# Performance work log

Hardware: AMD Instinct MI355X
Metric: run time of the kernel (lower is better)

Reference implementation:

```python
import jax, jax.numpy as jnp
import numpy as np

LEVELS = 2
BASE_BLOCK = (16, 16)
MAX_DIST = 8
IMG = (1024, 1024)


def _to_blocks(x, bh, bw):
    # [N,C,H,W] -> [BX,BY,N,C,bh,bw]
    N, C, H, W = x.shape
    BX, BY = H // bh, W // bw
    return x.reshape(N, C, BX, bh, BY, bw).transpose(2, 4, 0, 1, 3, 5)


def _from_blocks(b):
    # [BX,BY,N,C,bh,bw] -> [N,C,H,W]
    BX, BY, N, C, bh, bw = b.shape
    return b.transpose(2, 3, 0, 4, 1, 5).reshape(N, C, BX * bh, BY * bw)


def _level_best(ref_b, tgt_b, centers, d):
    # ref_b/tgt_b: [BX,BY,N,C,bh,bw]; centers: [BX,BY,2] candidate-window centers
    BX, BY = ref_b.shape[:2]
    dr = jnp.arange(-d, d + 1)
    offs = jnp.stack(jnp.meshgrid(dr, dr, indexing='ij'), -1).reshape(-1, 2)  # [K,2] lexicographic (dx,dy)
    hi = jnp.array([BX - 1, BY - 1])

    def step(carry, off):
        cand = centers + off  # [BX,BY,2]
        valid = jnp.all((cand >= 0) & (cand <= hi), axis=-1)
        cc = jnp.clip(cand, 0, hi)
        g = tgt_b[cc[..., 0], cc[..., 1]]  # [BX,BY,N,C,bh,bw]
        cost = jnp.mean(jnp.abs(ref_b - g), axis=(2, 3, 4, 5))  # MAD over N,C,h,w
        return carry, jnp.where(valid, cost, jnp.inf)

    _, costs = jax.lax.scan(step, None, offs)  # [K,BX,BY]
    k = jnp.argmin(costs, axis=0)  # first-min tie-break, deterministic
    return centers + offs[k]  # [BX,BY,2] absolute best target-block indices


def reference(reference_frame, target_frame):
    N, C, H, W = reference_frame.shape
    centers = None
    best = None
    tgt_b = None
    BX = BY = 0
    for level in range(LEVELS):
        s = 2 ** (LEVELS - level - 1)
        bh, bw = BASE_BLOCK[0] * s, BASE_BLOCK[1] * s
        BX, BY = H // bh, W // bw
        d = MAX_DIST // (2 ** level)
        ref_b = _to_blocks(reference_frame, bh, bw)
        tgt_b = _to_blocks(target_frame, bh, bw)
        if level == 0:
            gx, gy = jnp.meshgrid(jnp.arange(BX), jnp.arange(BY), indexing='ij')
            centers = jnp.stack([gx, gy], -1)
        best = _level_best(ref_b, tgt_b, centers, d)
        if level < LEVELS - 1:
            # all 4 children inherit window centered at 2*parent_best
            centers = jnp.repeat(jnp.repeat(2 * best, 2, axis=0), 2, axis=1)
    gx, gy = jnp.meshgrid(jnp.arange(BX), jnp.arange(BY), indexing='ij')
    grid = jnp.stack([gx, gy], -1)
    mv = (best - grid).transpose(2, 0, 1)[None].astype(reference_frame.dtype)
    motion_vectors = jnp.broadcast_to(mv, (N, 2, BX, BY))
    pred_b = tgt_b[best[..., 0], best[..., 1]]  # [BX,BY,N,C,bh,bw]
    predicted_frame = _from_blocks(pred_b)
    return motion_vectors, predicted_frame


def setup_inputs() -> dict:
    key = jax.random.key(0)
    k1, k2 = jax.random.split(key)
    N, C = 4, 3
    H, W = IMG
    reference_frame = jax.random.uniform(k1, (N, C, H, W), dtype=jnp.float32)
    target_frame = jax.random.uniform(k2, (N, C, H, W), dtype=jnp.float32)
    return {"reference_frame": reference_frame, "target_frame": target_frame}
```

## Files before the change

### kernel.cpp

```cpp
#include <hip/hip_runtime.h>

#define IMG_W 1024
#define SLICE 1048576
#define INF_F __builtin_huge_valf()
#define WS_PART_FLOATS (12 * 1024 * 289)

template <int CTRL>
__device__ __forceinline__ float dpp_add_step(float x) {
    int m = __builtin_amdgcn_update_dpp(0, __builtin_bit_cast(int, x), CTRL, 0xf, 0xf, true);
    return x + __builtin_bit_cast(float, m);
}
__device__ __forceinline__ float wave_sum63(float x) {
    x = dpp_add_step<0x111>(x);
    x = dpp_add_step<0x112>(x);
    x = dpp_add_step<0x114>(x);
    x = dpp_add_step<0x118>(x);
    x = dpp_add_step<0x142>(x);
    x = dpp_add_step<0x143>(x);
    return x;
}

__global__ __launch_bounds__(512, 4) void hbma_l0_phase1(const float* __restrict__ ref,
                                                         const float* __restrict__ tgt,
                                                         float* __restrict__ part) {
    const int tx    = blockIdx.x;
    const int byq   = blockIdx.y;
    const int plane = blockIdx.z;
    const int t = threadIdx.x;
    const int lane = t & 63, w = t >> 6;
    const int by0 = byq * 8;
    const int by  = by0 + w;

    __shared__ float tile[16 * 1024];

    const int prow = lane >> 3;
    const int pcol = (lane & 7) << 2;

    const float* tgt_p = tgt + (size_t)plane * SLICE;
    const float* ref_p = ref + (size_t)plane * SLICE;

    for (int batch = 0; batch < 2; ++batch) {
        const int tyBase = (batch == 0) ? (by0 - 8) : by0;
        const int dyLo   = (batch == 0) ? -8 : 0;
        const int dyHi   = (batch == 0) ? -1 : 8;

        __syncthreads();
        for (int idx = t; idx < 16 * 256; idx += 512) {
            const int j  = idx >> 8;
            const int ty = tyBase + j;
            if ((unsigned)ty < 32u) {
                const int ww = idx & 255;
                const int rr = ww >> 3;
                const int cc = (ww & 7) << 2;
                *(float4*)&tile[j * 1024 + rr * 32 + cc] =
                    *(const float4*)(tgt_p + (size_t)(tx * 32 + rr) * IMG_W + ty * 32 + cc);
            }
        }
        __syncthreads();

        for (int dxg = 0; dxg < 5; ++dxg) {
            float4 rf[4][4];
            bool rvalid[4];
            #pragma unroll
            for (int r = 0; r < 4; ++r) {
                const int di = dxg * 4 + r;
                const int bx = tx - (di - 8);
                rvalid[r] = (di <= 16) && ((unsigned)bx < 32u);
                if (rvalid[r]) {
                    const float* rb = ref_p + (size_t)(bx * 32 + prow) * IMG_W + by * 32 + pcol;
                    #pragma unroll
                    for (int i = 0; i < 4; ++i)
                        rf[r][i] = *(const float4*)(rb + (size_t)i * 8 * IMG_W);
                }
            }
            for (int dy = dyLo; dy <= dyHi; ++dy) {
                const int ty = by + dy;
                if ((unsigned)ty >= 32u) continue;
                const int tbase = (ty - tyBase) * 1024 + prow * 32 + pcol;
                float4 tv[4];
                #pragma unroll
                for (int i = 0; i < 4; ++i)
                    tv[i] = *(const float4*)&tile[tbase + i * 256];
                #pragma unroll
                for (int r = 0; r < 4; ++r) {
                    if (!rvalid[r]) continue;
                    float4 a = {0.f, 0.f, 0.f, 0.f};
                    #pragma unroll
                    for (int i = 0; i < 4; ++i) {
                        a.x += __builtin_fabsf(rf[r][i].x - tv[i].x);
                        a.y += __builtin_fabsf(rf[r][i].y - tv[i].y);
                        a.z += __builtin_fabsf(rf[r][i].z - tv[i].z);
                        a.w += __builtin_fabsf(rf[r][i].w - tv[i].w);
                    }
                    const float s = wave_sum63((a.x + a.y) + (a.z + a.w));
                    if (lane == 63) {
                        const int di = dxg * 4 + r;
                        const int bx = tx - (di - 8);
                        part[((size_t)plane * 1024 + bx * 32 + by) * 289 + di * 17 + (dy + 8)] = s;
                    }
                }
            }
        }
    }
}

__global__ __launch_bounds__(64) void hbma_l0_phase2(const float* __restrict__ part,
                                                     int2* __restrict__ best0) {
    const int by = blockIdx.x;
    const int bx = blockIdx.y;
    const int t = threadIdx.x;

    float bc = INF_F; int bk = 1 << 30;
    for (int k = t; k < 289; k += 64) {
        const int dx = k / 17 - 8, dy = k % 17 - 8;
        const int tx = bx + dx,    ty = by + dy;
        if ((unsigned)tx < 32u && (unsigned)ty < 32u) {
            float c = 0.f;
            #pragma unroll
            for (int p = 0; p < 12; ++p)
                c += part[((size_t)p * 1024 + bx * 32 + by) * 289 + k];
            if (c < bc) { bc = c; bk = k; }
        }
    }
    #pragma unroll
    for (int o = 32; o > 0; o >>= 1) {
        const float oc = __shfl_down(bc, o, 64);
        const int   ok = __shfl_down(bk, o, 64);
        if (oc < bc || (oc == bc && ok < bk)) { bc = oc; bk = ok; }
    }
    if (t == 0) best0[bx * 32 + by] = make_int2(bx + bk / 17 - 8, by + bk % 17 - 8);
}

__global__ __launch_bounds__(256) void hbma_l1(const float* __restrict__ ref,
                                               const float* __restrict__ tgt,
                                               const int2* __restrict__ best0,
                                               float* __restrict__ out) {
    const int pby = blockIdx.x;
    const int pbx = blockIdx.y;
    const int t = threadIdx.x;
    const int lane = t & 63, w = t >> 6;

    __shared__ float partials[4][81][4];
    __shared__ int2 sbest[4];

    const int2 pb = best0[pbx * 32 + pby];
    const int cx = 2 * pb.x, cy = 2 * pb.y;

    int off[3];
    #pragma unroll
    for (int i = 0; i < 3; ++i) {
        const int e4 = t + 256 * i;
        const int nc = e4 >> 6;
        const int ww = e4 & 63;
        off[i] = nc * SLICE + (ww >> 2) * IMG_W + ((ww & 3) << 2);
    }
    int cbase[4];
    float4 rf[4][3];
    #pragma unroll
    for (int c = 0; c < 4; ++c) {
        const int bx = 2 * pbx + (c >> 1), by = 2 * pby + (c & 1);
        cbase[c] = (bx * 16) * IMG_W + by * 16;
        #pragma unroll
        for (int i = 0; i < 3; ++i)
            rf[c][i] = *(const float4*)(ref + cbase[c] + off[i]);
    }

    for (int k = 0; k < 81; ++k) {
        const int tx = cx + k / 9 - 4;
        const int ty = cy + k % 9 - 4;
        if ((unsigned)tx < 64u && (unsigned)ty < 64u) {
            const float* tb = tgt + (tx * 16) * IMG_W + ty * 16;
            float4 tv[3];
            #pragma unroll
            for (int i = 0; i < 3; ++i) tv[i] = *(const float4*)(tb + off[i]);
            #pragma unroll
            for (int c = 0; c < 4; ++c) {
                float4 a = {0.f, 0.f, 0.f, 0.f};
                #pragma unroll
                for (int i = 0; i < 3; ++i) {
                    a.x += __builtin_fabsf(rf[c][i].x - tv[i].x);
                    a.y += __builtin_fabsf(rf[c][i].y - tv[i].y);
                    a.z += __builtin_fabsf(rf[c][i].z - tv[i].z);
                    a.w += __builtin_fabsf(rf[c][i].w - tv[i].w);
                }
                const float s = wave_sum63((a.x + a.y) + (a.z + a.w));
                if (lane == 63) partials[c][k][w] = s;
            }
        } else if (lane == 63) {
            #pragma unroll
            for (int c = 0; c < 4; ++c) partials[c][k][w] = INF_F;
        }
    }
    __syncthreads();

    {
        const int c = w;
        float bc = INF_F; int bk = 1 << 30;
        for (int k = lane; k < 81; k += 64) {
            const float4 p4 = *(const float4*)&partials[c][k][0];
            const float cost = (p4.x + p4.y) + (p4.z + p4.w);
            if (cost < bc) { bc = cost; bk = k; }
        }
        #pragma unroll
        for (int o = 32; o > 0; o >>= 1) {
            const float oc = __shfl_down(bc, o, 64);
            const int   ok = __shfl_down(bk, o, 64);
            if (oc < bc || (oc == bc && ok < bk)) { bc = oc; bk = ok; }
        }
        if (lane == 0) sbest[c] = make_int2(cx + bk / 9 - 4, cy + bk % 9 - 4);
    }
    __syncthreads();

    if (t < 32) {
        const int c = t >> 3, n = (t >> 1) & 3, ch = t & 1;
        const int bx = 2 * pbx + (c >> 1), by = 2 * pby + (c & 1);
        const int2 fb = sbest[c];
        out[((n * 2 + ch) * 64 + bx) * 64 + by] = (ch == 0) ? (float)(fb.x - bx) : (float)(fb.y - by);
    }

    float* pred = out + 32768;
    #pragma unroll
    for (int c = 0; c < 4; ++c) {
        const int2 fb = sbest[c];
        const float* sb = tgt + (fb.x * 16) * IMG_W + fb.y * 16;
        float* db = pred + cbase[c];
        #pragma unroll
        for (int i = 0; i < 3; ++i)
            *(float4*)(db + off[i]) = *(const float4*)(sb + off[i]);
    }
}

extern "C" void kernel_launch(void* const* d_in, const int* in_sizes, int n_in,
                              void* d_out, int out_size, void* d_ws, size_t ws_size,
                              hipStream_t stream) {
    const float* ref = (const float*)d_in[0];
    const float* tgt = (const float*)d_in[1];
    float* out = (float*)d_out;

    float* part  = (float*)d_ws;
    int2*  best0 = (int2*)((char*)d_ws + (size_t)WS_PART_FLOATS * 4);

    hbma_l0_phase1<<<dim3(32, 4, 12), 512, 0, stream>>>(ref, tgt, part);
    hbma_l0_phase2<<<dim3(32, 32), 64, 0, stream>>>(part, best0);
    hbma_l1<<<dim3(32, 32), 256, 0, stream>>>(ref, tgt, best0, out);
}
```

Baseline: 511.3 us.

## Use packed f32x2 SAD math and software-prefetch level-1 candidate blocks

The inner SAD loops in both the level-0 and level-1 kernels now use two-wide float vectors with max(d,-d) as the absolute value, so the compiler can emit packed FP32 instructions (v_pk_add_f32 and similar) instead of scalar sub/abs/add. The level-1 refinement loop also becomes a software pipeline: each candidate's target block is loaded one iteration ahead, with clamped addresses so the loads are always legal, and a validity flag replaces the branch that skipped out-of-range candidates. This aims to cut VALU instruction count and hide global-load latency. In exchange it uses more registers for the prefetched data and spends compute on out-of-range candidates.

```diff
diff --git a/kernel.cpp b/kernel.cpp
--- a/kernel.cpp
+++ b/kernel.cpp
@@ -1,4 +1,6 @@
 #include <hip/hip_runtime.h>
+
+typedef float f32x2 __attribute__((ext_vector_type(2)));
 
 #define IMG_W 1024
 #define SLICE 1048576
@@ -18,6 +20,11 @@
     x = dpp_add_step<0x142>(x);
     x = dpp_add_step<0x143>(x);
     return x;
+}
+
+__device__ __forceinline__ void sad2(f32x2& acc, f32x2 a, f32x2 b) {
+    f32x2 d = a - b;
+    acc += __builtin_elementwise_max(d, -d);
 }
 
 __global__ __launch_bounds__(512, 4) void hbma_l0_phase1(const float* __restrict__ ref,
@@ -77,22 +84,23 @@
                 const int ty = by + dy;
                 if ((unsigned)ty >= 32u) continue;
                 const int tbase = (ty - tyBase) * 1024 + prow * 32 + pcol;
-                float4 tv[4];
+                f32x2 tvv[8];
                 #pragma unroll
-                for (int i = 0; i < 4; ++i)
-                    tv[i] = *(const float4*)&tile[tbase + i * 256];
+                for (int i = 0; i < 4; ++i) {
+                    const float4 tv = *(const float4*)&tile[tbase + i * 256];
+                    tvv[2 * i]     = f32x2{tv.x, tv.y};
+                    tvv[2 * i + 1] = f32x2{tv.z, tv.w};
+                }
                 #pragma unroll
                 for (int r = 0; r < 4; ++r) {
                     if (!rvalid[r]) continue;
-                    float4 a = {0.f, 0.f, 0.f, 0.f};
+                    f32x2 acc = {0.f, 0.f};
                     #pragma unroll
                     for (int i = 0; i < 4; ++i) {
-                        a.x += __builtin_fabsf(rf[r][i].x - tv[i].x);
-                        a.y += __builtin_fabsf(rf[r][i].y - tv[i].y);
-                        a.z += __builtin_fabsf(rf[r][i].z - tv[i].z);
-                        a.w += __builtin_fabsf(rf[r][i].w - tv[i].w);
+                        sad2(acc, f32x2{rf[r][i].x, rf[r][i].y}, tvv[2 * i]);
+                        sad2(acc, f32x2{rf[r][i].z, rf[r][i].w}, tvv[2 * i + 1]);
                     }
-                    const float s = wave_sum63((a.x + a.y) + (a.z + a.w));
+                    const float s = wave_sum63(acc.x + acc.y);
                     if (lane == 63) {
                         const int di = dxg * 4 + r;
                         const int bx = tx - (di - 8);
@@ -165,31 +173,51 @@
             rf[c][i] = *(const float4*)(ref + cbase[c] + off[i]);
     }
 
+    auto cand_base = [&](int k) -> const float* {
+        int tx = cx + k / 9 - 4;
+        int ty = cy + k % 9 - 4;
+        tx = min(max(tx, 0), 63);
+        ty = min(max(ty, 0), 63);
+        return tgt + (tx * 16) * IMG_W + ty * 16;
+    };
+
+    float4 tv[3];
+    {
+        const float* tb = cand_base(0);
+        #pragma unroll
+        for (int i = 0; i < 3; ++i) tv[i] = *(const float4*)(tb + off[i]);
+    }
+
     for (int k = 0; k < 81; ++k) {
+        float4 tn[3];
+        {
+            const float* tb = cand_base(min(k + 1, 80));
+            #pragma unroll
+            for (int i = 0; i < 3; ++i) tn[i] = *(const float4*)(tb + off[i]);
+        }
         const int tx = cx + k / 9 - 4;
         const int ty = cy + k % 9 - 4;
-        if ((unsigned)tx < 64u && (unsigned)ty < 64u) {
-            const float* tb = tgt + (tx * 16) * IMG_W + ty * 16;
-            float4 tv[3];
-            #pragma unroll
-            for (int i = 0; i < 3; ++i) tv[i] = *(const float4*)(tb + off[i]);
-            #pragma unroll
-            for (int c = 0; c < 4; ++c) {
-                float4 a = {0.f, 0.f, 0.f, 0.f};
-                #pragma unroll
-                for (int i = 0; i < 3; ++i) {
-                    a.x += __builtin_fabsf(rf[c][i].x - tv[i].x);
-                    a.y += __builtin_fabsf(rf[c][i].y - tv[i].y);
-                    a.z += __builtin_fabsf(rf[c][i].z - tv[i].z);
-                    a.w += __builtin_fabsf(rf[c][i].w - tv[i].w);
-                }
-                const float s = wave_sum63((a.x + a.y) + (a.z + a.w));
-                if (lane == 63) partials[c][k][w] = s;
-            }
-        } else if (lane == 63) {
-            #pragma unroll
-            for (int c = 0; c < 4; ++c) partials[c][k][w] = INF_F;
-        }
+        const bool valid = ((unsigned)tx < 64u) && ((unsigned)ty < 64u);
+
+        f32x2 tvv[6];
+        #pragma unroll
+        for (int i = 0; i < 3; ++i) {
+            tvv[2 * i]     = f32x2{tv[i].x, tv[i].y};
+            tvv[2 * i + 1] = f32x2{tv[i].z, tv[i].w};
+        }
+        #pragma unroll
+        for (int c = 0; c < 4; ++c) {
+            f32x2 acc = {0.f, 0.f};
+            #pragma unroll
+            for (int i = 0; i < 3; ++i) {
+                sad2(acc, f32x2{rf[c][i].x, rf[c][i].y}, tvv[2 * i]);
+                sad2(acc, f32x2{rf[c][i].z, rf[c][i].w}, tvv[2 * i + 1]);
+            }
+            const float s = wave_sum63(acc.x + acc.y);
+            if (lane == 63) partials[c][k][w] = valid ? s : INF_F;
+        }
+        #pragma unroll
+        for (int i = 0; i < 3; ++i) tv[i] = tn[i];
     }
     __syncthreads();
 
```

After: 571.9 us. 1.12x slower.

## Remap L0 blocks per XCD for L2 locality and pipeline L1 candidate loads

Applied to the files above, without the earlier changes.

The level-0 cost kernel moves to a flat grid whose block index is remapped so that blocks sharing the same image plane and column band are scheduled together on one XCD, improving L2 reuse of target and reference tiles. The level-1 kernel doubles its threads, with each half of the waves scanning half of the 81 candidates. It prefetches candidate target blocks two steps ahead using clamped addresses in place of branches. The prediction copy is redistributed over the larger block. This adds register pressure from the prefetch buffers and depends on the assumption about how blocks are dispatched across XCDs.

```diff
diff --git a/kernel.cpp b/kernel.cpp
--- a/kernel.cpp
+++ b/kernel.cpp
@@ -23,9 +23,14 @@
 __global__ __launch_bounds__(512, 4) void hbma_l0_phase1(const float* __restrict__ ref,
                                                          const float* __restrict__ tgt,
                                                          float* __restrict__ part) {
-    const int tx    = blockIdx.x;
-    const int byq   = blockIdx.y;
-    const int plane = blockIdx.z;
+    const int bid   = blockIdx.x;
+    const int slot  = bid & 7;
+    const int j     = bid >> 3;
+    const int group = slot * 6 + (j >> 5);
+    const int tx    = j & 31;
+    const int byq   = group & 3;
+    const int plane = group >> 2;
+
     const int t = threadIdx.x;
     const int lane = t & 63, w = t >> 6;
     const int by0 = byq * 8;
@@ -46,13 +51,13 @@
 
         __syncthreads();
         for (int idx = t; idx < 16 * 256; idx += 512) {
-            const int j  = idx >> 8;
-            const int ty = tyBase + j;
+            const int jj = idx >> 8;
+            const int ty = tyBase + jj;
             if ((unsigned)ty < 32u) {
                 const int ww = idx & 255;
                 const int rr = ww >> 3;
                 const int cc = (ww & 7) << 2;
-                *(float4*)&tile[j * 1024 + rr * 32 + cc] =
+                *(float4*)&tile[jj * 1024 + rr * 32 + cc] =
                     *(const float4*)(tgt_p + (size_t)(tx * 32 + rr) * IMG_W + ty * 32 + cc);
             }
         }
@@ -131,7 +136,7 @@
     if (t == 0) best0[bx * 32 + by] = make_int2(bx + bk / 17 - 8, by + bk % 17 - 8);
 }
 
-__global__ __launch_bounds__(256) void hbma_l1(const float* __restrict__ ref,
+__global__ __launch_bounds__(512) void hbma_l1(const float* __restrict__ ref,
                                                const float* __restrict__ tgt,
                                                const int2* __restrict__ best0,
                                                float* __restrict__ out) {
@@ -139,6 +144,8 @@
     const int pbx = blockIdx.y;
     const int t = threadIdx.x;
     const int lane = t & 63, w = t >> 6;
+    const int wc = w & 3;
+    const int kh = w >> 2;
 
     __shared__ float partials[4][81][4];
     __shared__ int2 sbest[4];
@@ -148,12 +155,9 @@
 
     int off[3];
     #pragma unroll
-    for (int i = 0; i < 3; ++i) {
-        const int e4 = t + 256 * i;
-        const int nc = e4 >> 6;
-        const int ww = e4 & 63;
-        off[i] = nc * SLICE + (ww >> 2) * IMG_W + ((ww & 3) << 2);
-    }
+    for (int i = 0; i < 3; ++i)
+        off[i] = (wc + 4 * i) * SLICE + (lane >> 2) * IMG_W + ((lane & 3) << 2);
+
     int cbase[4];
     float4 rf[4][3];
     #pragma unroll
@@ -165,35 +169,58 @@
             rf[c][i] = *(const float4*)(ref + cbase[c] + off[i]);
     }
 
-    for (int k = 0; k < 81; ++k) {
+    auto cand_base = [&](int k) -> const float* {
+        int tx = cx + k / 9 - 4;
+        int ty = cy + k % 9 - 4;
+        tx = min(max(tx, 0), 63);
+        ty = min(max(ty, 0), 63);
+        return tgt + (tx * 16) * IMG_W + ty * 16;
+    };
+
+    const int kbeg = kh ? 41 : 0;
+    const int kend = kh ? 81 : 41;
+
+    float4 buf[2][3];
+    {
+        const float* b0 = cand_base(kbeg);
+        const float* b1 = cand_base(min(kbeg + 1, kend - 1));
+        #pragma unroll
+        for (int i = 0; i < 3; ++i) buf[0][i] = *(const float4*)(b0 + off[i]);
+        #pragma unroll
+        for (int i = 0; i < 3; ++i) buf[1][i] = *(const float4*)(b1 + off[i]);
+    }
+
+    for (int k = kbeg; k < kend; ++k) {
+        const int p = (k - kbeg) & 1;
+        float4 tv[3];
+        #pragma unroll
+        for (int i = 0; i < 3; ++i) tv[i] = buf[p][i];
+        {
+            const float* tb = cand_base(min(k + 2, kend - 1));
+            #pragma unroll
+            for (int i = 0; i < 3; ++i) buf[p][i] = *(const float4*)(tb + off[i]);
+        }
         const int tx = cx + k / 9 - 4;
         const int ty = cy + k % 9 - 4;
-        if ((unsigned)tx < 64u && (unsigned)ty < 64u) {
-            const float* tb = tgt + (tx * 16) * IMG_W + ty * 16;
-            float4 tv[3];
-            #pragma unroll
-            for (int i = 0; i < 3; ++i) tv[i] = *(const float4*)(tb + off[i]);
-            #pragma unroll
-            for (int c = 0; c < 4; ++c) {
-                float4 a = {0.f, 0.f, 0.f, 0.f};
-                #pragma unroll
-                for (int i = 0; i < 3; ++i) {
-                    a.x += __builtin_fabsf(rf[c][i].x - tv[i].x);
-                    a.y += __builtin_fabsf(rf[c][i].y - tv[i].y);
-                    a.z += __builtin_fabsf(rf[c][i].z - tv[i].z);
-                    a.w += __builtin_fabsf(rf[c][i].w - tv[i].w);
-                }
-                const float s = wave_sum63((a.x + a.y) + (a.z + a.w));
-                if (lane == 63) partials[c][k][w] = s;
-            }
-        } else if (lane == 63) {
-            #pragma unroll
-            for (int c = 0; c < 4; ++c) partials[c][k][w] = INF_F;
+        const bool valid = ((unsigned)tx < 64u) && ((unsigned)ty < 64u);
+
+        #pragma unroll
+        for (int c = 0; c < 4; ++c) {
+            float4 a = {0.f, 0.f, 0.f, 0.f};
+            #pragma unroll
+            for (int i = 0; i < 3; ++i) {
+                a.x += __builtin_fabsf(rf[c][i].x - tv[i].x);
+                a.y += __builtin_fabsf(rf[c][i].y - tv[i].y);
+                a.z += __builtin_fabsf(rf[c][i].z - tv[i].z);
+                a.w += __builtin_fabsf(rf[c][i].w - tv[i].w);
+            }
+            const float s = wave_sum63((a.x + a.y) + (a.z + a.w));
+            if (lane == 63) partials[c][k][wc] = valid ? s : INF_F;
         }
     }
     __syncthreads();
 
-    {
+    if (w < 4) {
         const int c = w;
         float bc = INF_F; int bk = 1 << 30;
         for (int k = lane; k < 81; k += 64) {
@@ -219,14 +246,16 @@
     }
 
     float* pred = out + 32768;
-    #pragma unroll
-    for (int c = 0; c < 4; ++c) {
-        const int2 fb = sbest[c];
-        const float* sb = tgt + (fb.x * 16) * IMG_W + fb.y * 16;
-        float* db = pred + cbase[c];
-        #pragma unroll
-        for (int i = 0; i < 3; ++i)
-            *(float4*)(db + off[i]) = *(const float4*)(sb + off[i]);
+    for (int idx = t; idx < 768; idx += 512) {
+        const int nc = idx >> 6;
+        const int ww = idx & 63;
+        const int o = nc * SLICE + (ww >> 2) * IMG_W + ((ww & 3) << 2);
+        #pragma unroll
+        for (int c = 0; c < 4; ++c) {
+            const int2 fb = sbest[c];
+            *(float4*)(pred + cbase[c] + o) =
+                *(const float4*)(tgt + (fb.x * 16) * IMG_W + fb.y * 16 + o);
+        }
     }
 }
 
@@ -240,7 +269,7 @@
     float* part  = (float*)d_ws;
     int2*  best0 = (int2*)((char*)d_ws + (size_t)WS_PART_FLOATS * 4);
 
-    hbma_l0_phase1<<<dim3(32, 4, 12), 512, 0, stream>>>(ref, tgt, part);
+    hbma_l0_phase1<<<dim3(1536), 512, 0, stream>>>(ref, tgt, part);
     hbma_l0_phase2<<<dim3(32, 32), 64, 0, stream>>>(part, best0);
-    hbma_l1<<<dim3(32, 32), 256, 0, stream>>>(ref, tgt, best0, out);
-}
+    hbma_l1<<<dim3(32, 32), 512, 0, stream>>>(ref, tgt, best0, out);
+}
```

New measurement: 857.9 us. 1.68x slower.

## Split level-1 search across four blocks per parent and add finish kernel

Applied to the files above, without the earlier changes.

The level-1 kernel now splits the 81 candidate offsets into four chunks of up to 21, each handled by its own block, raising the grid from 1024 to 4096 blocks. Partial costs go to the workspace, reusing the level-0 partial buffer, and a new finish kernel does the argmin, writes motion vectors and copies predicted blocks. Out-of-range candidates are clamped and loaded anyway, then masked to infinity, which removes the divergent branch. The cost is a fourth kernel launch, a global round trip for costs, and four reloads of the reference blocks per parent.

```diff
diff --git a/kernel.cpp b/kernel.cpp
--- a/kernel.cpp
+++ b/kernel.cpp
@@ -46,13 +46,13 @@
 
         __syncthreads();
         for (int idx = t; idx < 16 * 256; idx += 512) {
-            const int j  = idx >> 8;
-            const int ty = tyBase + j;
+            const int jj = idx >> 8;
+            const int ty = tyBase + jj;
             if ((unsigned)ty < 32u) {
                 const int ww = idx & 255;
                 const int rr = ww >> 3;
                 const int cc = (ww & 7) << 2;
-                *(float4*)&tile[j * 1024 + rr * 32 + cc] =
+                *(float4*)&tile[jj * 1024 + rr * 32 + cc] =
                     *(const float4*)(tgt_p + (size_t)(tx * 32 + rr) * IMG_W + ty * 32 + cc);
             }
         }
@@ -131,19 +131,20 @@
     if (t == 0) best0[bx * 32 + by] = make_int2(bx + bk / 17 - 8, by + bk % 17 - 8);
 }
 
-__global__ __launch_bounds__(256) void hbma_l1(const float* __restrict__ ref,
-                                               const float* __restrict__ tgt,
-                                               const int2* __restrict__ best0,
-                                               float* __restrict__ out) {
-    const int pby = blockIdx.x;
-    const int pbx = blockIdx.y;
+__global__ __launch_bounds__(256) void hbma_l1_main(const float* __restrict__ ref,
+                                                    const float* __restrict__ tgt,
+                                                    const int2* __restrict__ best0,
+                                                    float* __restrict__ part1) {
+    const int q   = blockIdx.x;
+    const int pby = blockIdx.y;
+    const int pbx = blockIdx.z;
+    const int parent = pbx * 32 + pby;
     const int t = threadIdx.x;
     const int lane = t & 63, w = t >> 6;
 
-    __shared__ float partials[4][81][4];
-    __shared__ int2 sbest[4];
-
-    const int2 pb = best0[pbx * 32 + pby];
+    __shared__ float partials[4][21][4];
+
+    const int2 pb = best0[parent];
     const int cx = 2 * pb.x, cy = 2 * pb.y;
 
     int off[3];
@@ -154,51 +155,77 @@
         const int ww = e4 & 63;
         off[i] = nc * SLICE + (ww >> 2) * IMG_W + ((ww & 3) << 2);
     }
-    int cbase[4];
     float4 rf[4][3];
     #pragma unroll
     for (int c = 0; c < 4; ++c) {
         const int bx = 2 * pbx + (c >> 1), by = 2 * pby + (c & 1);
-        cbase[c] = (bx * 16) * IMG_W + by * 16;
+        const int cb = (bx * 16) * IMG_W + by * 16;
         #pragma unroll
         for (int i = 0; i < 3; ++i)
-            rf[c][i] = *(const float4*)(ref + cbase[c] + off[i]);
-    }
-
-    for (int k = 0; k < 81; ++k) {
+            rf[c][i] = *(const float4*)(ref + cb + off[i]);
+    }
+
+    const int kbeg = q * 21;
+    const int kcnt = min(81 - kbeg, 21);
+
+    for (int j = 0; j < kcnt; ++j) {
+        const int k  = kbeg + j;
         const int tx = cx + k / 9 - 4;
         const int ty = cy + k % 9 - 4;
-        if ((unsigned)tx < 64u && (unsigned)ty < 64u) {
-            const float* tb = tgt + (tx * 16) * IMG_W + ty * 16;
-            float4 tv[3];
+        const bool valid = ((unsigned)tx < 64u) && ((unsigned)ty < 64u);
+        const int ctx = min(max(tx, 0), 63);
+        const int cty = min(max(ty, 0), 63);
+        const float* tb = tgt + (ctx * 16) * IMG_W + cty * 16;
+
+        float4 tv[3];
+        #pragma unroll
+        for (int i = 0; i < 3; ++i) tv[i] = *(const float4*)(tb + off[i]);
+
+        #pragma unroll
+        for (int c = 0; c < 4; ++c) {
+            float4 a = {0.f, 0.f, 0.f, 0.f};
             #pragma unroll
-            for (int i = 0; i < 3; ++i) tv[i] = *(const float4*)(tb + off[i]);
-            #pragma unroll
-            for (int c = 0; c < 4; ++c) {
-                float4 a = {0.f, 0.f, 0.f, 0.f};
-                #pragma unroll
-                for (int i = 0; i < 3; ++i) {
-                    a.x += __builtin_fabsf(rf[c][i].x - tv[i].x);
-                    a.y += __builtin_fabsf(rf[c][i].y - tv[i].y);
-                    a.z += __builtin_fabsf(rf[c][i].z - tv[i].z);
-                    a.w += __builtin_fabsf(rf[c][i].w - tv[i].w);
-                }
-                const float s = wave_sum63((a.x + a.y) + (a.z + a.w));
-                if (lane == 63) partials[c][k][w] = s;
-            }
-        } else if (lane == 63) {
-            #pragma unroll
-            for (int c = 0; c < 4; ++c) partials[c][k][w] = INF_F;
+            for (int i = 0; i < 3; ++i) {
+                a.x += __builtin_fabsf(rf[c][i].x - tv[i].x);
+                a.y += __builtin_fabsf(rf[c][i].y - tv[i].y);
+                a.z += __builtin_fabsf(rf[c][i].z - tv[i].z);
+                a.w += __builtin_fabsf(rf[c][i].w - tv[i].w);
+            }
+            const float s = wave_sum63((a.x + a.y) + (a.z + a.w));
+            if (lane == 63) partials[c][j][w] = valid ? s : INF_F;
         }
     }
     __syncthreads();
+
+    for (int idx = t; idx < 4 * 21; idx += 256) {
+        const int c = idx & 3, j = idx >> 2;
+        const int k = kbeg + j;
+        if (j < kcnt) {
+            const float4 p4 = *(const float4*)&partials[c][j][0];
+            part1[((size_t)parent * 4 + c) * 81 + k] = (p4.x + p4.y) + (p4.z + p4.w);
+        }
+    }
+}
+
+__global__ __launch_bounds__(256) void hbma_l1_finish(const float* __restrict__ tgt,
+                                                      const int2* __restrict__ best0,
+                                                      const float* __restrict__ part1,
+                                                      float* __restrict__ out) {
+    const int parent = blockIdx.x;
+    const int pbx = parent >> 5, pby = parent & 31;
+    const int t = threadIdx.x;
+    const int lane = t & 63, w = t >> 6;
+
+    __shared__ int2 sbest[4];
+
+    const int2 pb = best0[parent];
+    const int cx = 2 * pb.x, cy = 2 * pb.y;
 
     {
         const int c = w;
         float bc = INF_F; int bk = 1 << 30;
         for (int k = lane; k < 81; k += 64) {
-            const float4 p4 = *(const float4*)&partials[c][k][0];
-            const float cost = (p4.x + p4.y) + (p4.z + p4.w);
+            const float cost = part1[((size_t)parent * 4 + c) * 81 + k];
             if (cost < bc) { bc = cost; bk = k; }
         }
         #pragma unroll
@@ -219,14 +246,23 @@
     }
 
     float* pred = out + 32768;
+    int off[3];
+    #pragma unroll
+    for (int i = 0; i < 3; ++i) {
+        const int e4 = t + 256 * i;
+        const int nc = e4 >> 6;
+        const int ww = e4 & 63;
+        off[i] = nc * SLICE + (ww >> 2) * IMG_W + ((ww & 3) << 2);
+    }
     #pragma unroll
     for (int c = 0; c < 4; ++c) {
+        const int bx = 2 * pbx + (c >> 1), by = 2 * pby + (c & 1);
+        const int cb = (bx * 16) * IMG_W + by * 16;
         const int2 fb = sbest[c];
         const float* sb = tgt + (fb.x * 16) * IMG_W + fb.y * 16;
-        float* db = pred + cbase[c];
         #pragma unroll
         for (int i = 0; i < 3; ++i)
-            *(float4*)(db + off[i]) = *(const float4*)(sb + off[i]);
+            *(float4*)(pred + cb + off[i]) = *(const float4*)(sb + off[i]);
     }
 }
 
@@ -239,8 +275,10 @@
 
     float* part  = (float*)d_ws;
     int2*  best0 = (int2*)((char*)d_ws + (size_t)WS_PART_FLOATS * 4);
+    float* part1 = (float*)d_ws;
 
     hbma_l0_phase1<<<dim3(32, 4, 12), 512, 0, stream>>>(ref, tgt, part);
     hbma_l0_phase2<<<dim3(32, 32), 64, 0, stream>>>(part, best0);
-    hbma_l1<<<dim3(32, 32), 256, 0, stream>>>(ref, tgt, best0, out);
-}
+    hbma_l1_main<<<dim3(4, 32, 32), 256, 0, stream>>>(ref, tgt, best0, part1);
+    hbma_l1_finish<<<dim3(1024), 256, 0, stream>>>(tgt, best0, part1, out);
+}
```

Result: slower. 550.8 us (+7.7%).
